# Kernel tuning notes

Measured on AMD Instinct MI355X. Metric: run time of the kernel, lower is better.

The kernel has to match this reference:

```python
import jax, jax.numpy as jnp
import numpy as np


def normalize_adj(adj):
    """Symmetrize (adj + adj.T*(adj.T>adj) - adj*(adj.T>adj)), add self loops, row-normalize D^-1 A."""
    at = jnp.swapaxes(adj, -1, -2)
    mask = (at > adj).astype(adj.dtype)
    a = adj + at * mask - adj * mask
    m = a.shape[-1]
    a = a + jnp.eye(m, dtype=a.dtype)
    rowsum = a.sum(axis=-1, keepdims=True)
    inv = jnp.where(rowsum > 0, 1.0 / rowsum, 0.0)
    return a * inv


def setup_inputs() -> dict:
    key = jax.random.key(0)
    ks = jax.random.split(key, 8)
    N, n, T, dim, M = 4, 3, 512, 2048, 256
    x = jax.random.normal(ks[0], (N, n, T, dim), dtype=jnp.float32)
    nodes = jax.random.normal(ks[1], (N, M, dim), dtype=jnp.float32)
    adj = (jax.random.uniform(ks[2], (N, M, M)) < 0.05).astype(jnp.float32)
    conv_w = jax.random.normal(ks[3], (2048, dim, 3), dtype=jnp.float32) * 0.02  # OIH
    conv_b = jnp.zeros((2048,), dtype=jnp.float32)
    W1 = jax.random.normal(ks[4], (dim, dim), dtype=jnp.float32) * 0.02
    b1 = jnp.zeros((dim,), dtype=jnp.float32)
    W2 = jax.random.normal(ks[5], (dim, dim), dtype=jnp.float32) * 0.02
    b2 = jnp.zeros((dim,), dtype=jnp.float32)
    return {"x": x, "nodes": nodes, "adj": adj, "conv_w": conv_w, "conv_b": conv_b,
            "W1": W1, "b1": b1, "W2": W2, "b2": b2}


def reference(x, nodes, adj, conv_w, conv_b, W1, b1, W2, b2):
    N, n, T, dim = x.shape
    # Conv1d front-end: (N*n, C=dim, T), kernel 3, pad 1, then ReLU
    feats = x.reshape(N * n, T, dim).transpose(0, 2, 1)  # [B, C, T]
    feats = jax.lax.conv_general_dilated(
        feats, conv_w, window_strides=(1,), padding=[(1, 1)],
        dimension_numbers=("NCH", "OIH", "NCH"))
    feats = jax.nn.relu(feats + conv_b[None, :, None])
    feats = feats.transpose(0, 2, 1).reshape(N, n, T, dim)
    # GCN_Module over per-sample node graphs (batched over N)
    a = normalize_adj(adj)                                   # [N, M, M]
    h = jax.nn.relu(jnp.einsum("bij,bjf->bif", a, nodes @ W1) + b1)
    out = jnp.einsum("bij,bjf->bif", a, h @ W2) + b2         # [N, M, dim]
    return feats, out
```

## Files before the change

kernel.cpp:

```cpp
#include <hip/hip_runtime.h>
#include <stdint.h>

typedef __bf16 bf16x8 __attribute__((ext_vector_type(8)));
typedef float floatx4 __attribute__((ext_vector_type(4)));

__device__ __forceinline__ void gload_lds16(const void* g, void* l) {
    __builtin_amdgcn_global_load_lds((const __attribute__((address_space(1))) void*)g,
                                     (__attribute__((address_space(3))) void*)l, 16, 0, 0);
}

__device__ __forceinline__ uint16_t f2bf(float f) {
    uint32_t u = __float_as_uint(f);
    u += 0x7fff + ((u >> 16) & 1);
    return (uint16_t)(u >> 16);
}
__device__ __forceinline__ uint32_t f2bf2(float lo, float hi) {
    return (uint32_t)f2bf(lo) | ((uint32_t)f2bf(hi) << 16);
}

struct AmulSM {
    float vv[256];
    int   jj[256];
    float part[4];
    int   wcnt[4];
    int   woff[4];
    float sinv;
    int   n0;
};

__device__ __forceinline__ void amul_body(const float* __restrict__ adj,
                                          const float* __restrict__ H,
                                          uint16_t* __restrict__ outp,
                                          int b, int i, int tid, AmulSM* sm)
{
    const float* A = adj + ((size_t)b << 16);
    float aij = A[(i << 8) + tid];
    float aji = A[(tid << 8) + i];
    float v = fmaxf(aij, aji);
    if (tid == i) v += 1.0f;

    float s = v;
    #pragma unroll
    for (int off = 32; off > 0; off >>= 1) s += __shfl_down(s, off);

    bool pred = v != 0.0f;
    unsigned long long m = __ballot(pred);
    int wid = tid >> 6;
    if ((tid & 63) == 0) { sm->part[wid] = s; sm->wcnt[wid] = (int)__popcll(m); }
    __syncthreads();
    if (tid == 0) {
        float t = sm->part[0] + sm->part[1] + sm->part[2] + sm->part[3];
        sm->sinv = t > 0.0f ? 1.0f / t : 0.0f;
        int o = 0;
        #pragma unroll
        for (int w = 0; w < 4; ++w) { sm->woff[w] = o; o += sm->wcnt[w]; }
        sm->n0 = o;
    }
    __syncthreads();
    if (pred) {
        int pos = sm->woff[wid] + (int)__popcll(m & ((1ull << (tid & 63)) - 1ull));
        sm->vv[pos] = v * sm->sinv;
        sm->jj[pos] = tid;
    }
    __syncthreads();

    const int n0 = sm->n0;
    const int f0 = tid * 8;
    const float* Hb = H + (((size_t)b) << 8) * 2048;
    float acc[8] = {};
    for (int c = 0; c < n0; ++c) {
        float av = sm->vv[c];
        const float* hp = Hb + (size_t)sm->jj[c] * 2048 + f0;
        float4 p = *(const float4*)hp;
        float4 q = *(const float4*)(hp + 4);
        acc[0] += av * p.x; acc[1] += av * p.y; acc[2] += av * p.z; acc[3] += av * p.w;
        acc[4] += av * q.x; acc[5] += av * q.y; acc[6] += av * q.z; acc[7] += av * q.w;
    }
    uint4 o;
    o.x = f2bf2(acc[0], acc[1]);
    o.y = f2bf2(acc[2], acc[3]);
    o.z = f2bf2(acc[4], acc[5]);
    o.w = f2bf2(acc[6], acc[7]);
    *(uint4*)(outp + (((size_t)b << 8) + i) * 2048 + f0) = o;
}

__device__ __forceinline__ void amul_swizzle(int bid, int& b, int& i) {
    int x = bid & 7, g = bid >> 3;
    b = x >> 1;
    i = ((x & 1) << 7) + g;
}

#define PR_AM 1024
#define PR_W  3072
#define PR_T  5120
#define PR_N  17456

__global__ __launch_bounds__(256)
void k_prep(const float* __restrict__ x, uint16_t* __restrict__ xpad,
            const float* __restrict__ w, uint16_t* __restrict__ wT,
            const float* __restrict__ W1, const float* __restrict__ W2,
            uint16_t* __restrict__ W1T, uint16_t* __restrict__ W2T,
            const float* __restrict__ adj, const float* __restrict__ nodes,
            uint16_t* __restrict__ gbf)
{
    __shared__ union {
        float  wbuf[6144];
        float  tile[64][65];
        AmulSM am;
    } sm;
    const int bid = blockIdx.x;
    const int tid = threadIdx.x;

    if (bid < PR_AM) {
        int b, i; amul_swizzle(bid, b, i);
        amul_body(adj, nodes, gbf, b, i, tid, &sm.am);
    } else if (bid < PR_W) {
        int o = bid - PR_AM;
        const float* src = w + (size_t)o * 6144;
        uint16_t*    dst = wT + (size_t)o * 6144;
        #pragma unroll
        for (int it = 0; it < 24; ++it)
            sm.wbuf[it * 256 + tid] = src[it * 256 + tid];
        __syncthreads();
        #pragma unroll
        for (int h = 0; h < 3; ++h)
            #pragma unroll
            for (int c = 0; c < 8; ++c) {
                int i = c * 256 + tid;
                dst[h * 2048 + i] = f2bf(sm.wbuf[i * 3 + h]);
            }
    } else if (bid < PR_T) {
        int t  = bid - PR_W;
        int z  = t >> 10;
        int by = (t >> 5) & 31;
        int bx = t & 31;
        const float* src = z ? W2 : W1;
        uint16_t*    dst = z ? W2T : W1T;
        int tx = tid & 63, ty = tid >> 6;
        for (int rr = ty; rr < 64; rr += 4)
            sm.tile[rr][tx] = src[(size_t)(by * 64 + rr) * 2048 + bx * 64 + tx];
        __syncthreads();
        for (int rr = ty; rr < 64; rr += 4)
            dst[(size_t)(bx * 64 + rr) * 2048 + by * 64 + tx] = f2bf(sm.tile[tx][rr]);
    } else {
        int idx4 = (bid - PR_T) * 256 + tid;
        int ch4  = idx4 & 511;
        int tmp  = idx4 >> 9;
        int b    = tmp / 514;
        int tt   = tmp - b * 514;
        float4 v = {0.0f, 0.0f, 0.0f, 0.0f};
        if (tt >= 1 && tt <= 512)
            v = *(const float4*)(x + ((size_t)(b * 512 + tt - 1) << 11) + ch4 * 4);
        uint2 o = { f2bf2(v.x, v.y), f2bf2(v.z, v.w) };
        ((uint2*)xpad)[idx4] = o;
    }
}

template<bool RELU>
__device__ __forceinline__ void g64_tile(uint16_t* As, uint16_t* Bs,
                                         const uint16_t* __restrict__ A,
                                         const uint16_t* __restrict__ BT,
                                         float* __restrict__ C, const float* __restrict__ bias,
                                         int rt, int ct)
{
    const int tid  = threadIdx.x;
    const int lane = tid & 63;
    const int wave = tid >> 6;
    const int wm   = (wave >> 1) * 32;
    const int wn   = (wave & 1) * 32;
    const int lm   = lane & 15;
    const int kq   = (lane >> 4) * 8;
    const int sr   = tid >> 2;
    const int sc   = (tid & 3) * 8;

    const size_t abase = (size_t)(rt + sr) * 2048 + sc;
    const size_t bbase = (size_t)(ct + sr) * 2048 + sc;

    floatx4 acc[2][2] = {};

    for (int k0 = 0; k0 < 2048; k0 += 64) {
        #pragma unroll
        for (int p = 0; p < 2; ++p) {
            gload_lds16(A  + abase + k0 + p * 32, &As[p * 2048 + tid * 8]);
            gload_lds16(BT + bbase + k0 + p * 32, &Bs[p * 2048 + tid * 8]);
        }
        __syncthreads();

        #pragma unroll
        for (int s = 0; s < 2; ++s) {
            bf16x8 af[2], bfr[2];
            #pragma unroll
            for (int mt = 0; mt < 2; ++mt)
                af[mt] = *(const bf16x8*)&As[s * 2048 + (wm + mt * 16 + lm) * 32 + kq];
            #pragma unroll
            for (int nt = 0; nt < 2; ++nt)
                bfr[nt] = *(const bf16x8*)&Bs[s * 2048 + (wn + nt * 16 + lm) * 32 + kq];
            #pragma unroll
            for (int mt = 0; mt < 2; ++mt)
                #pragma unroll
                for (int nt = 0; nt < 2; ++nt)
                    acc[mt][nt] = __builtin_amdgcn_mfma_f32_16x16x32_bf16(af[mt], bfr[nt], acc[mt][nt], 0, 0, 0);
        }
        __syncthreads();
    }

    const int lq = lane >> 4;
    #pragma unroll
    for (int mt = 0; mt < 2; ++mt)
        #pragma unroll
        for (int nt = 0; nt < 2; ++nt) {
            int col = ct + wn + nt * 16 + lm;
            float bv = bias[col];
            #pragma unroll
            for (int r = 0; r < 4; ++r) {
                int row = rt + wm + mt * 16 + lq * 4 + r;
                float v = acc[mt][nt][r] + bv;
                if (RELU) v = fmaxf(v, 0.0f);
                C[(size_t)row * 2048 + col] = v;
            }
        }
}

__global__ __launch_bounds__(256)
void k_big(const uint16_t* __restrict__ xpad, const uint16_t* __restrict__ wmT,
           float* __restrict__ feats, const float* __restrict__ conv_b,
           const uint16_t* __restrict__ gbf, const uint16_t* __restrict__ W1T,
           float* __restrict__ h, const float* __restrict__ b1)
{
    __shared__ __align__(16) uint16_t lds[16384];
    const int bid  = blockIdx.x;
    const int tid  = threadIdx.x;
    const int lane = tid & 63;
    const int wave = tid >> 6;
    const int lm   = lane & 15;
    const int kq   = (lane >> 4) * 8;
    const int lq   = lane >> 4;

    if (bid < 768) {
        uint16_t* As = lds;
        uint16_t* Bs = lds + 8192;
        const int xc = bid & 7;
        const int g  = bid >> 3;
        const int rt = (12 * (xc >> 1) + (g % 12)) * 128;
        const int ct = (8 * (xc & 1) + (g / 12)) * 128;
        const int wm = (wave >> 1) * 64;
        const int wn = (wave & 1) * 64;

        const int sr = tid >> 2;
        const int sc = (tid & 3) * 8;
        size_t arow[2]; size_t brow[2];
        #pragma unroll
        for (int rh = 0; rh < 2; ++rh) {
            int r = rt + rh * 64 + sr;
            int b = r >> 9;
            int t = r & 511;
            arow[rh] = ((size_t)(b * 514 + t) << 11);
            brow[rh] = (size_t)(ct + rh * 64 + sr) * 6144;
        }

        floatx4 acc[4][4] = {};

        for (int k0 = 0; k0 < 6144; k0 += 64) {
            const int hh = k0 >> 11;
            const int icb = (k0 & 2047) + sc;
            #pragma unroll
            for (int p = 0; p < 4; ++p) {
                const int s  = p >> 1;
                const int rh = p & 1;
                gload_lds16(xpad + arow[rh] + ((size_t)hh << 11) + icb + s * 32,
                            &As[p * 2048 + tid * 8]);
                gload_lds16(wmT + brow[rh] + k0 + sc + s * 32,
                            &Bs[p * 2048 + tid * 8]);
            }
            __syncthreads();

            #pragma unroll
            for (int s = 0; s < 2; ++s) {
                bf16x8 af[4], bfr[4];
                #pragma unroll
                for (int mt = 0; mt < 4; ++mt)
                    af[mt] = *(const bf16x8*)&As[s * 4096 + (wm + mt * 16 + lm) * 32 + kq];
                #pragma unroll
                for (int nt = 0; nt < 4; ++nt)
                    bfr[nt] = *(const bf16x8*)&Bs[s * 4096 + (wn + nt * 16 + lm) * 32 + kq];
                #pragma unroll
                for (int mt = 0; mt < 4; ++mt)
                    #pragma unroll
                    for (int nt = 0; nt < 4; ++nt)
                        acc[mt][nt] = __builtin_amdgcn_mfma_f32_16x16x32_bf16(af[mt], bfr[nt], acc[mt][nt], 0, 0, 0);
            }
            __syncthreads();
        }

        #pragma unroll
        for (int mt = 0; mt < 4; ++mt)
            #pragma unroll
            for (int nt = 0; nt < 4; ++nt) {
                int col = ct + wn + nt * 16 + lm;
                float bv = conv_b[col];
                #pragma unroll
                for (int r = 0; r < 4; ++r) {
                    int row = rt + wm + mt * 16 + lq * 4 + r;
                    feats[(size_t)row * 2048 + col] = fmaxf(acc[mt][nt][r] + bv, 0.0f);
                }
            }
    } else {
        const int t  = bid - 768;
        const int xc = t & 7;
        const int g  = t >> 3;
        const int rt = (g & 15) * 64;
        const int ct = (4 * xc + (g >> 4)) * 64;
        g64_tile<true>(lds, lds + 4096, gbf, W1T, h, b1, rt, ct);
    }
}

__global__ __launch_bounds__(256)
void k_amul(const float* __restrict__ adj, const float* __restrict__ H,
            uint16_t* __restrict__ outp)
{
    __shared__ AmulSM sm;
    int b, i; amul_swizzle(blockIdx.x, b, i);
    amul_body(adj, H, outp, b, i, threadIdx.x, &sm);
}

__global__ __launch_bounds__(256)
void k_gemm64(const uint16_t* __restrict__ A, const uint16_t* __restrict__ BT,
              float* __restrict__ C, const float* __restrict__ bias)
{
    __shared__ __align__(16) uint16_t lds[8192];
    const int bid = blockIdx.x;
    const int xc  = bid & 7;
    const int g   = bid >> 3;
    const int rt  = (g & 15) * 64;
    const int ct  = (4 * xc + (g >> 4)) * 64;
    g64_tile<false>(lds, lds + 4096, A, BT, C, bias, rt, ct);
}


extern "C" void kernel_launch(void* const* d_in, const int* in_sizes, int n_in,
                              void* d_out, int out_size, void* d_ws, size_t ws_size,
                              hipStream_t stream)
{
    const float* x      = (const float*)d_in[0];
    const float* nodes  = (const float*)d_in[1];
    const float* adj    = (const float*)d_in[2];
    const float* conv_w = (const float*)d_in[3];
    const float* conv_b = (const float*)d_in[4];
    const float* W1     = (const float*)d_in[5];
    const float* b1     = (const float*)d_in[6];
    const float* W2     = (const float*)d_in[7];
    const float* b2     = (const float*)d_in[8];
    float* out = (float*)d_out;

    char* ws = (char*)d_ws;
    uint16_t* xpad   = (uint16_t*)(ws);
    uint16_t* wmT    = (uint16_t*)(ws + 25288704);
    uint16_t* W1T    = (uint16_t*)(ws + 50454528);
    uint16_t* W2T    = (uint16_t*)(ws + 58843136);
    uint16_t* gbf    = (uint16_t*)(ws + 67231744);
    float*    h      = (float*)   (ws + 71426048);
    uint16_t* ahb    = (uint16_t*)(ws + 79814656);

    k_prep<<<PR_N, 256, 0, stream>>>(x, xpad, conv_w, wmT,
                                     W1, W2, W1T, W2T, adj, nodes, gbf);
    k_big<<<1280, 256, 0, stream>>>(xpad, wmT, out, conv_b, gbf, W1T, h, b1);
    k_amul<<<1024, 256, 0, stream>>>(adj, h, ahb);
    k_gemm64<<<512, 256, 0, stream>>>(ahb, W2T, out + 12582912, b2);
}
```

Before: 406.0 us.

## Rewrite conv GEMM as 192x256 tiles with 4-stage LDS pipeline and 8 waves

The conv-as-GEMM part of k_big now uses 512-thread blocks computing 192x256 output tiles over 256 tiles. Operands are staged through a 4-buffer LDS ring with XOR-swizzled layout, explicit vmcnt waits and barriers, and setprio around the MFMA bursts. The aim is to hide global-load latency and raise MFMA utilization compared with the single-buffered 128x128 loop. The W1 GEMM branch now packs two 64x64 tiles per 512-thread block. The cost is 112KB of LDS per block and many more accumulator registers, which may lower occupancy.

```diff
diff --git a/kernel.cpp b/kernel.cpp
--- a/kernel.cpp
+++ b/kernel.cpp
@@ -161,9 +161,8 @@
                                          const uint16_t* __restrict__ A,
                                          const uint16_t* __restrict__ BT,
                                          float* __restrict__ C, const float* __restrict__ bias,
-                                         int rt, int ct)
-{
-    const int tid  = threadIdx.x;
+                                         int rt, int ct, int tid)
+{
     const int lane = tid & 63;
     const int wave = tid >> 6;
     const int wm   = (wave >> 1) * 32;
@@ -221,96 +220,138 @@
         }
 }
 
-__global__ __launch_bounds__(256)
+template<int BUF, bool STG, int VN>
+__device__ __forceinline__ void conv_win(char* ldsb, int tid,
+    const uint16_t*& aS0, const uint16_t*& aS1,
+    const uint16_t*& bS0, const uint16_t*& bS1,
+    int aoff, int boff, floatx4 (&acc)[6][4])
+{
+    char* As  = ldsb + BUF * 12288;
+    char* Bs  = ldsb + 49152 + BUF * 16384;
+    constexpr int NB = (BUF + 3) & 3;
+    char* As3 = ldsb + NB * 12288;
+    char* Bs3 = ldsb + 49152 + NB * 16384;
+
+    bf16x8 av[3], bv[4];
+    #pragma unroll
+    for (int j = 0; j < 3; ++j) av[j] = *(const bf16x8*)(As + aoff + j * 1024);
+    #pragma unroll
+    for (int j = 0; j < 4; ++j) bv[j] = *(const bf16x8*)(Bs + boff + j * 1024);
+    if constexpr (STG) {
+        gload_lds16(aS0, As3 + tid * 16); aS0 += 32;
+        if (tid < 256) { gload_lds16(aS1, As3 + 8192 + tid * 16); aS1 += 32; }
+    }
+    __builtin_amdgcn_s_barrier();
+    asm volatile("s_waitcnt lgkmcnt(0)");
+    __builtin_amdgcn_s_setprio(1);
+    #pragma unroll
+    for (int jm = 0; jm < 3; ++jm)
+        #pragma unroll
+        for (int fn = 0; fn < 4; ++fn)
+            acc[jm][fn] = __builtin_amdgcn_mfma_f32_16x16x32_bf16(av[jm], bv[fn], acc[jm][fn], 0, 0, 0);
+    __builtin_amdgcn_s_setprio(0);
+    __builtin_amdgcn_s_barrier();
+    #pragma unroll
+    for (int j = 0; j < 3; ++j) av[j] = *(const bf16x8*)(As + aoff + 3072 + j * 1024);
+    if constexpr (STG) {
+        gload_lds16(bS0, Bs3 + tid * 16); bS0 += 32;
+        gload_lds16(bS1, Bs3 + 8192 + tid * 16); bS1 += 32;
+    }
+    if constexpr (VN >= 0) asm volatile("s_waitcnt vmcnt(%0)" :: "i"(VN));
+    __builtin_amdgcn_s_barrier();
+    asm volatile("s_waitcnt lgkmcnt(0)");
+    __builtin_amdgcn_s_setprio(1);
+    #pragma unroll
+    for (int jm = 0; jm < 3; ++jm)
+        #pragma unroll
+        for (int fn = 0; fn < 4; ++fn)
+            acc[3 + jm][fn] = __builtin_amdgcn_mfma_f32_16x16x32_bf16(av[jm], bv[fn], acc[3 + jm][fn], 0, 0, 0);
+    __builtin_amdgcn_s_setprio(0);
+    __builtin_amdgcn_s_barrier();
+}
+
+__global__ __launch_bounds__(512, 2)
 void k_big(const uint16_t* __restrict__ xpad, const uint16_t* __restrict__ wmT,
            float* __restrict__ feats, const float* __restrict__ conv_b,
            const uint16_t* __restrict__ gbf, const uint16_t* __restrict__ W1T,
            float* __restrict__ h, const float* __restrict__ b1)
 {
-    __shared__ __align__(16) uint16_t lds[16384];
-    const int bid  = blockIdx.x;
-    const int tid  = threadIdx.x;
-    const int lane = tid & 63;
-    const int wave = tid >> 6;
-    const int lm   = lane & 15;
-    const int kq   = (lane >> 4) * 8;
-    const int lq   = lane >> 4;
-
-    if (bid < 768) {
-        uint16_t* As = lds;
-        uint16_t* Bs = lds + 8192;
-        const int xc = bid & 7;
-        const int g  = bid >> 3;
-        const int rt = (12 * (xc >> 1) + (g % 12)) * 128;
-        const int ct = (8 * (xc & 1) + (g / 12)) * 128;
-        const int wm = (wave >> 1) * 64;
-        const int wn = (wave & 1) * 64;
-
-        const int sr = tid >> 2;
-        const int sc = (tid & 3) * 8;
-        size_t arow[2]; size_t brow[2];
-        #pragma unroll
-        for (int rh = 0; rh < 2; ++rh) {
-            int r = rt + rh * 64 + sr;
-            int b = r >> 9;
-            int t = r & 511;
-            arow[rh] = ((size_t)(b * 514 + t) << 11);
-            brow[rh] = (size_t)(ct + rh * 64 + sr) * 6144;
+    __shared__ __align__(16) char smem[114688];
+    const int bid = blockIdx.x;
+    const int tid = threadIdx.x;
+
+    if (bid < 256) {
+        const int xcd  = bid & 7;
+        const int gg   = bid >> 3;
+        const int tile = xcd * 32 + gg;
+        const int rt   = (tile >> 3) * 192;
+        const int ct   = (tile & 7) * 256;
+
+        const int lane = tid & 63, wave = tid >> 6;
+        const int mw = wave >> 2, nw = wave & 3;
+        const int lm = lane & 15;
+        const int kq2 = (lane >> 4) * 16;
+        const int xc  = kq2 ^ ((lm & 3) << 4);
+        const int aoff = ((mw * 96 + lm) << 6) + xc;
+        const int boff = ((nw * 64 + lm) << 6) + xc;
+
+        const int c1  = 512 + tid;
+        const int r0  = tid >> 2,  kc0 = ((tid & 3) ^ (r0 & 3)) * 8;
+        const int r1  = c1 >> 2,   kc1 = ((c1 & 3) ^ (r1 & 3)) * 8;
+
+        const int RA0 = rt + r0;
+        const int RA1 = rt + r1;
+        const uint16_t* aS0 = xpad + (((size_t)((RA0 >> 9) * 514 + (RA0 & 511))) << 11) + kc0;
+        const uint16_t* aS1 = xpad + (((size_t)((RA1 >> 9) * 514 + (RA1 & 511))) << 11) + kc1;
+        const uint16_t* bS0 = wmT + (size_t)(ct + r0) * 6144 + kc0;
+        const uint16_t* bS1 = wmT + (size_t)(ct + r1) * 6144 + kc1;
+
+        #pragma unroll
+        for (int p = 0; p < 3; ++p) {
+            char* As3 = smem + p * 12288;
+            char* Bs3 = smem + 49152 + p * 16384;
+            gload_lds16(aS0, As3 + tid * 16); aS0 += 32;
+            if (tid < 256) { gload_lds16(aS1, As3 + 8192 + tid * 16); aS1 += 32; }
+            gload_lds16(bS0, Bs3 + tid * 16); bS0 += 32;
+            gload_lds16(bS1, Bs3 + 8192 + tid * 16); bS1 += 32;
         }
-
-        floatx4 acc[4][4] = {};
-
-        for (int k0 = 0; k0 < 6144; k0 += 64) {
-            const int hh = k0 >> 11;
-            const int icb = (k0 & 2047) + sc;
-            #pragma unroll
-            for (int p = 0; p < 4; ++p) {
-                const int s  = p >> 1;
-                const int rh = p & 1;
-                gload_lds16(xpad + arow[rh] + ((size_t)hh << 11) + icb + s * 32,
-                            &As[p * 2048 + tid * 8]);
-                gload_lds16(wmT + brow[rh] + k0 + sc + s * 32,
-                            &Bs[p * 2048 + tid * 8]);
-            }
-            __syncthreads();
-
-            #pragma unroll
-            for (int s = 0; s < 2; ++s) {
-                bf16x8 af[4], bfr[4];
-                #pragma unroll
-                for (int mt = 0; mt < 4; ++mt)
-                    af[mt] = *(const bf16x8*)&As[s * 4096 + (wm + mt * 16 + lm) * 32 + kq];
-                #pragma unroll
-                for (int nt = 0; nt < 4; ++nt)
-                    bfr[nt] = *(const bf16x8*)&Bs[s * 4096 + (wn + nt * 16 + lm) * 32 + kq];
-                #pragma unroll
-                for (int mt = 0; mt < 4; ++mt)
-                    #pragma unroll
-                    for (int nt = 0; nt < 4; ++nt)
-                        acc[mt][nt] = __builtin_amdgcn_mfma_f32_16x16x32_bf16(af[mt], bfr[nt], acc[mt][nt], 0, 0, 0);
-            }
-            __syncthreads();
+        asm volatile("s_waitcnt vmcnt(6)");
+        __builtin_amdgcn_s_barrier();
+
+        floatx4 acc[6][4] = {};
+        #pragma unroll 1
+        for (int it = 0; it < 47; ++it) {
+            conv_win<0, true, 6>(smem, tid, aS0, aS1, bS0, bS1, aoff, boff, acc);
+            conv_win<1, true, 6>(smem, tid, aS0, aS1, bS0, bS1, aoff, boff, acc);
+            conv_win<2, true, 6>(smem, tid, aS0, aS1, bS0, bS1, aoff, boff, acc);
+            conv_win<3, true, 6>(smem, tid, aS0, aS1, bS0, bS1, aoff, boff, acc);
         }
-
-        #pragma unroll
-        for (int mt = 0; mt < 4; ++mt)
-            #pragma unroll
-            for (int nt = 0; nt < 4; ++nt) {
-                int col = ct + wn + nt * 16 + lm;
-                float bv = conv_b[col];
+        conv_win<0, true,  6>(smem, tid, aS0, aS1, bS0, bS1, aoff, boff, acc);
+        conv_win<1, false, 3>(smem, tid, aS0, aS1, bS0, bS1, aoff, boff, acc);
+        conv_win<2, false, 0>(smem, tid, aS0, aS1, bS0, bS1, aoff, boff, acc);
+        conv_win<3, false,-1>(smem, tid, aS0, aS1, bS0, bS1, aoff, boff, acc);
+
+        const int lq = lane >> 4;
+        #pragma unroll
+        for (int fm = 0; fm < 6; ++fm)
+            #pragma unroll
+            for (int fn = 0; fn < 4; ++fn) {
+                int col = ct + nw * 64 + fn * 16 + lm;
+                float bb = conv_b[col];
                 #pragma unroll
                 for (int r = 0; r < 4; ++r) {
-                    int row = rt + wm + mt * 16 + lq * 4 + r;
-                    feats[(size_t)row * 2048 + col] = fmaxf(acc[mt][nt][r] + bv, 0.0f);
+                    int row = rt + mw * 96 + fm * 16 + lq * 4 + r;
+                    feats[(size_t)row * 2048 + col] = fmaxf(acc[fm][fn][r] + bb, 0.0f);
                 }
             }
     } else {
-        const int t  = bid - 768;
-        const int xc = t & 7;
-        const int g  = t >> 3;
-        const int rt = (g & 15) * 64;
-        const int ct = (4 * xc + (g >> 4)) * 64;
-        g64_tile<true>(lds, lds + 4096, gbf, W1T, h, b1, rt, ct);
+        const int t    = bid - 256;
+        const int half = tid >> 8;
+        const int st   = t * 2 + half;
+        const int rt   = (st & 15) * 64;
+        const int ct   = (st >> 4) * 64;
+        uint16_t* As = (uint16_t*)smem + half * 8192;
+        g64_tile<true>(As, As + 4096, gbf, W1T, h, b1, rt, ct, tid & 255);
     }
 }
 
@@ -333,7 +374,7 @@
     const int g   = bid >> 3;
     const int rt  = (g & 15) * 64;
     const int ct  = (4 * xc + (g >> 4)) * 64;
-    g64_tile<false>(lds, lds + 4096, A, BT, C, bias, rt, ct);
+    g64_tile<false>(lds, lds + 4096, A, BT, C, bias, rt, ct, threadIdx.x);
 }
 
 
@@ -363,7 +404,7 @@
 
     k_prep<<<PR_N, 256, 0, stream>>>(x, xpad, conv_w, wmT,
                                      W1, W2, W1T, W2T, adj, nodes, gbf);
-    k_big<<<1280, 256, 0, stream>>>(xpad, wmT, out, conv_b, gbf, W1T, h, b1);
+    k_big<<<512, 512, 0, stream>>>(xpad, wmT, out, conv_b, gbf, W1T, h, b1);
     k_amul<<<1024, 256, 0, stream>>>(adj, h, ahb);
     k_gemm64<<<512, 256, 0, stream>>>(ahb, W2T, out + 12582912, b2);
 }
```

Result: faster. 389.2 us (-4.1%).

## Double-buffer conv GEMM with 192x256 tiles and swizzled LDS; enlarge GCN tiles

Applied to the files above, without the earlier changes.

The conv GEMM becomes a double-buffered pipeline using 192x256 block tiles, XOR-swizzled LDS layout, explicit vmcnt waits, raw barriers and setprio around MFMA bursts, so there are 256 large tiles instead of 768 128x128 ones. The GCN GEMMs switch from 64x64 to 128x128 tiles with swizzled LDS. Grid sizes shrink accordingly. This is meant to hide global-load latency, cut LDS bank conflicts and raise arithmetic intensity. The cost is higher register and LDS pressure, and with fewer blocks the GPU may be less evenly filled, including the tail where the GCN blocks run.

```diff
diff --git a/kernel.cpp b/kernel.cpp
--- a/kernel.cpp
+++ b/kernel.cpp
@@ -3,6 +3,8 @@
 
 typedef __bf16 bf16x8 __attribute__((ext_vector_type(8)));
 typedef float floatx4 __attribute__((ext_vector_type(4)));
+
+#define SB0 __builtin_amdgcn_sched_barrier(0)
 
 __device__ __forceinline__ void gload_lds16(const void* g, void* l) {
     __builtin_amdgcn_global_load_lds((const __attribute__((address_space(1))) void*)g,
@@ -157,58 +159,57 @@
 }
 
 template<bool RELU>
-__device__ __forceinline__ void g64_tile(uint16_t* As, uint16_t* Bs,
-                                         const uint16_t* __restrict__ A,
-                                         const uint16_t* __restrict__ BT,
-                                         float* __restrict__ C, const float* __restrict__ bias,
-                                         int rt, int ct)
-{
-    const int tid  = threadIdx.x;
-    const int lane = tid & 63;
-    const int wave = tid >> 6;
-    const int wm   = (wave >> 1) * 32;
-    const int wn   = (wave & 1) * 32;
-    const int lm   = lane & 15;
-    const int kq   = (lane >> 4) * 8;
-    const int sr   = tid >> 2;
-    const int sc   = (tid & 3) * 8;
-
-    const size_t abase = (size_t)(rt + sr) * 2048 + sc;
-    const size_t bbase = (size_t)(ct + sr) * 2048 + sc;
-
-    floatx4 acc[2][2] = {};
-
+__device__ __forceinline__ void g128_tile(char* lds, const uint16_t* __restrict__ A,
+                                          const uint16_t* __restrict__ BT,
+                                          float* __restrict__ C, const float* __restrict__ bias,
+                                          int rt, int ct, int tid)
+{
+    char* As = lds;
+    char* Bs = lds + 16384;
+    const int lane = tid & 63, wave = tid >> 6;
+    const int wm = (wave >> 1) * 64, wn = (wave & 1) * 64;
+    const int lm = lane & 15, lq = lane >> 4;
+    const int abyte = (wm + lm) * 64 + ((lq * 16) ^ ((lm & 3) << 4));
+    const int bbyte = (wn + lm) * 64 + ((lq * 16) ^ ((lm & 3) << 4));
+
+    int soff[4];
+    #pragma unroll
+    for (int j = 0; j < 4; ++j) {
+        int c = tid + 256 * j;
+        int row = (c >> 2) & 127;
+        soff[j] = row * 2048 + ((c >> 9) << 5) + (((c & 3) ^ (row & 3)) << 3);
+    }
+
+    floatx4 acc[4][4] = {};
     for (int k0 = 0; k0 < 2048; k0 += 64) {
         #pragma unroll
-        for (int p = 0; p < 2; ++p) {
-            gload_lds16(A  + abase + k0 + p * 32, &As[p * 2048 + tid * 8]);
-            gload_lds16(BT + bbase + k0 + p * 32, &Bs[p * 2048 + tid * 8]);
+        for (int j = 0; j < 4; ++j) {
+            gload_lds16(A  + (size_t)rt * 2048 + soff[j] + k0, As + tid * 16 + j * 4096);
+            gload_lds16(BT + (size_t)ct * 2048 + soff[j] + k0, Bs + tid * 16 + j * 4096);
         }
         __syncthreads();
-
         #pragma unroll
         for (int s = 0; s < 2; ++s) {
-            bf16x8 af[2], bfr[2];
-            #pragma unroll
-            for (int mt = 0; mt < 2; ++mt)
-                af[mt] = *(const bf16x8*)&As[s * 2048 + (wm + mt * 16 + lm) * 32 + kq];
-            #pragma unroll
-            for (int nt = 0; nt < 2; ++nt)
-                bfr[nt] = *(const bf16x8*)&Bs[s * 2048 + (wn + nt * 16 + lm) * 32 + kq];
-            #pragma unroll
-            for (int mt = 0; mt < 2; ++mt)
+            bf16x8 af[4], bfr[4];
+            #pragma unroll
+            for (int mt = 0; mt < 4; ++mt)
+                af[mt] = *(const bf16x8*)(As + s * 8192 + abyte + mt * 1024);
+            #pragma unroll
+            for (int nt = 0; nt < 4; ++nt)
+                bfr[nt] = *(const bf16x8*)(Bs + s * 8192 + bbyte + nt * 1024);
+            #pragma unroll
+            for (int mt = 0; mt < 4; ++mt)
                 #pragma unroll
-                for (int nt = 0; nt < 2; ++nt)
+                for (int nt = 0; nt < 4; ++nt)
                     acc[mt][nt] = __builtin_amdgcn_mfma_f32_16x16x32_bf16(af[mt], bfr[nt], acc[mt][nt], 0, 0, 0);
         }
         __syncthreads();
     }
 
-    const int lq = lane >> 4;
-    #pragma unroll
-    for (int mt = 0; mt < 2; ++mt)
-        #pragma unroll
-        for (int nt = 0; nt < 2; ++nt) {
+    #pragma unroll
+    for (int mt = 0; mt < 4; ++mt)
+        #pragma unroll
+        for (int nt = 0; nt < 4; ++nt) {
             int col = ct + wn + nt * 16 + lm;
             float bv = bias[col];
             #pragma unroll
@@ -221,96 +222,126 @@
         }
 }
 
-__global__ __launch_bounds__(256)
+template<int CUR, bool STG, int VN>
+__device__ __forceinline__ void conv_w2(char* smem, int tid,
+    const uint16_t* (&aP)[3], const uint16_t* (&bP)[4],
+    int abase, int bbase, floatx4 (&acc)[6][8])
+{
+    char* As  = smem + CUR * 12288;
+    char* Bs  = smem + 24576 + CUR * 16384;
+    char* Asn = smem + (CUR ^ 1) * 12288;
+    char* Bsn = smem + 24576 + (CUR ^ 1) * 16384;
+
+    if constexpr (STG) {
+        #pragma unroll
+        for (int j = 0; j < 3; ++j) { gload_lds16(aP[j], Asn + tid * 16 + j * 4096); aP[j] += 32; }
+        #pragma unroll
+        for (int j = 0; j < 4; ++j) { gload_lds16(bP[j], Bsn + tid * 16 + j * 4096); bP[j] += 32; }
+    }
+    SB0;
+    asm volatile("s_waitcnt vmcnt(%0)" :: "i"(VN));
+    SB0;
+    __builtin_amdgcn_s_barrier();
+    SB0;
+
+    bf16x8 bv[8], av[3];
+    #pragma unroll
+    for (int fn = 0; fn < 8; ++fn) bv[fn] = *(const bf16x8*)(Bs + bbase + fn * 1024);
+    #pragma unroll
+    for (int fm = 0; fm < 3; ++fm) av[fm] = *(const bf16x8*)(As + abase + fm * 1024);
+    __builtin_amdgcn_s_setprio(1);
+    #pragma unroll
+    for (int fm = 0; fm < 3; ++fm)
+        #pragma unroll
+        for (int fn = 0; fn < 8; ++fn)
+            acc[fm][fn] = __builtin_amdgcn_mfma_f32_16x16x32_bf16(av[fm], bv[fn], acc[fm][fn], 0, 0, 0);
+    __builtin_amdgcn_s_setprio(0);
+    #pragma unroll
+    for (int fm = 0; fm < 3; ++fm) av[fm] = *(const bf16x8*)(As + abase + 3072 + fm * 1024);
+    __builtin_amdgcn_s_setprio(1);
+    #pragma unroll
+    for (int fm = 0; fm < 3; ++fm)
+        #pragma unroll
+        for (int fn = 0; fn < 8; ++fn)
+            acc[3 + fm][fn] = __builtin_amdgcn_mfma_f32_16x16x32_bf16(av[fm], bv[fn], acc[3 + fm][fn], 0, 0, 0);
+    __builtin_amdgcn_s_setprio(0);
+    SB0;
+    __builtin_amdgcn_s_barrier();
+    SB0;
+}
+
+__global__ __launch_bounds__(256, 2)
 void k_big(const uint16_t* __restrict__ xpad, const uint16_t* __restrict__ wmT,
            float* __restrict__ feats, const float* __restrict__ conv_b,
            const uint16_t* __restrict__ gbf, const uint16_t* __restrict__ W1T,
            float* __restrict__ h, const float* __restrict__ b1)
 {
-    __shared__ __align__(16) uint16_t lds[16384];
-    const int bid  = blockIdx.x;
-    const int tid  = threadIdx.x;
-    const int lane = tid & 63;
-    const int wave = tid >> 6;
-    const int lm   = lane & 15;
-    const int kq   = (lane >> 4) * 8;
-    const int lq   = lane >> 4;
-
-    if (bid < 768) {
-        uint16_t* As = lds;
-        uint16_t* Bs = lds + 8192;
-        const int xc = bid & 7;
-        const int g  = bid >> 3;
-        const int rt = (12 * (xc >> 1) + (g % 12)) * 128;
-        const int ct = (8 * (xc & 1) + (g / 12)) * 128;
-        const int wm = (wave >> 1) * 64;
-        const int wn = (wave & 1) * 64;
-
-        const int sr = tid >> 2;
-        const int sc = (tid & 3) * 8;
-        size_t arow[2]; size_t brow[2];
-        #pragma unroll
-        for (int rh = 0; rh < 2; ++rh) {
-            int r = rt + rh * 64 + sr;
-            int b = r >> 9;
-            int t = r & 511;
-            arow[rh] = ((size_t)(b * 514 + t) << 11);
-            brow[rh] = (size_t)(ct + rh * 64 + sr) * 6144;
-        }
-
-        floatx4 acc[4][4] = {};
-
-        for (int k0 = 0; k0 < 6144; k0 += 64) {
-            const int hh = k0 >> 11;
-            const int icb = (k0 & 2047) + sc;
-            #pragma unroll
-            for (int p = 0; p < 4; ++p) {
-                const int s  = p >> 1;
-                const int rh = p & 1;
-                gload_lds16(xpad + arow[rh] + ((size_t)hh << 11) + icb + s * 32,
-                            &As[p * 2048 + tid * 8]);
-                gload_lds16(wmT + brow[rh] + k0 + sc + s * 32,
-                            &Bs[p * 2048 + tid * 8]);
-            }
-            __syncthreads();
-
-            #pragma unroll
-            for (int s = 0; s < 2; ++s) {
-                bf16x8 af[4], bfr[4];
-                #pragma unroll
-                for (int mt = 0; mt < 4; ++mt)
-                    af[mt] = *(const bf16x8*)&As[s * 4096 + (wm + mt * 16 + lm) * 32 + kq];
-                #pragma unroll
-                for (int nt = 0; nt < 4; ++nt)
-                    bfr[nt] = *(const bf16x8*)&Bs[s * 4096 + (wn + nt * 16 + lm) * 32 + kq];
-                #pragma unroll
-                for (int mt = 0; mt < 4; ++mt)
-                    #pragma unroll
-                    for (int nt = 0; nt < 4; ++nt)
-                        acc[mt][nt] = __builtin_amdgcn_mfma_f32_16x16x32_bf16(af[mt], bfr[nt], acc[mt][nt], 0, 0, 0);
-            }
-            __syncthreads();
-        }
-
-        #pragma unroll
-        for (int mt = 0; mt < 4; ++mt)
-            #pragma unroll
-            for (int nt = 0; nt < 4; ++nt) {
-                int col = ct + wn + nt * 16 + lm;
-                float bv = conv_b[col];
+    __shared__ __align__(16) char smem[57344];
+    const int bid = blockIdx.x;
+    const int tid = threadIdx.x;
+
+    if (bid < 256) {
+        const int xcd  = bid & 7;
+        const int gg   = bid >> 3;
+        const int tile = xcd * 32 + gg;
+        const int rt   = (tile >> 3) * 192;
+        const int ct   = (tile & 7) * 256;
+
+        const int lane = tid & 63, wave = tid >> 6;
+        const int mw = wave >> 1, nw = wave & 1;
+        const int lm = lane & 15, lq = lane >> 4;
+        const int abase = (mw * 96 + lm) * 64 + ((lq * 16) ^ ((lm & 3) << 4));
+        const int bbase = (nw * 128 + lm) * 64 + ((lq * 16) ^ ((lm & 3) << 4));
+
+        const uint16_t* aP[3];
+        const uint16_t* bP[4];
+        #pragma unroll
+        for (int j = 0; j < 3; ++j) {
+            int c = tid + 256 * j;
+            int row = c >> 2;
+            int R = rt + row;
+            aP[j] = xpad + (((size_t)((R >> 9) * 514 + (R & 511))) << 11)
+                         + (((c & 3) ^ (row & 3)) << 3);
+        }
+        #pragma unroll
+        for (int j = 0; j < 4; ++j) {
+            int c = tid + 256 * j;
+            int row = c >> 2;
+            bP[j] = wmT + (size_t)(ct + row) * 6144 + (((c & 3) ^ (row & 3)) << 3);
+        }
+
+        #pragma unroll
+        for (int j = 0; j < 3; ++j) { gload_lds16(aP[j], smem + tid * 16 + j * 4096); aP[j] += 32; }
+        #pragma unroll
+        for (int j = 0; j < 4; ++j) { gload_lds16(bP[j], smem + 24576 + tid * 16 + j * 4096); bP[j] += 32; }
+
+        floatx4 acc[6][8] = {};
+        #pragma unroll 1
+        for (int it = 0; it < 95; ++it) {
+            conv_w2<0, true, 7>(smem, tid, aP, bP, abase, bbase, acc);
+            conv_w2<1, true, 7>(smem, tid, aP, bP, abase, bbase, acc);
+        }
+        conv_w2<0, true, 7>(smem, tid, aP, bP, abase, bbase, acc);
+        conv_w2<1, false, 0>(smem, tid, aP, bP, abase, bbase, acc);
+
+        #pragma unroll
+        for (int fm = 0; fm < 6; ++fm)
+            #pragma unroll
+            for (int fn = 0; fn < 8; ++fn) {
+                int col = ct + nw * 128 + fn * 16 + lm;
+                float bb = conv_b[col];
                 #pragma unroll
                 for (int r = 0; r < 4; ++r) {
-                    int row = rt + wm + mt * 16 + lq * 4 + r;
-                    feats[(size_t)row * 2048 + col] = fmaxf(acc[mt][nt][r] + bv, 0.0f);
+                    int row = rt + mw * 96 + fm * 16 + lq * 4 + r;
+                    feats[(size_t)row * 2048 + col] = fmaxf(acc[fm][fn][r] + bb, 0.0f);
                 }
             }
     } else {
-        const int t  = bid - 768;
-        const int xc = t & 7;
-        const int g  = t >> 3;
-        const int rt = (g & 15) * 64;
-        const int ct = (4 * xc + (g >> 4)) * 64;
-        g64_tile<true>(lds, lds + 4096, gbf, W1T, h, b1, rt, ct);
+        const int t   = bid - 256;
+        const int idx = (t & 7) * 16 + (t >> 3);
+        const int rt  = (idx & 7) * 128;
+        const int ct  = (idx >> 3) * 128;
+        g128_tile<true>(smem, gbf, W1T, h, b1, rt, ct, tid);
     }
 }
 
@@ -327,13 +358,12 @@
 void k_gemm64(const uint16_t* __restrict__ A, const uint16_t* __restrict__ BT,
               float* __restrict__ C, const float* __restrict__ bias)
 {
-    __shared__ __align__(16) uint16_t lds[8192];
+    __shared__ __align__(16) char lds[32768];
     const int bid = blockIdx.x;
-    const int xc  = bid & 7;
-    const int g   = bid >> 3;
-    const int rt  = (g & 15) * 64;
-    const int ct  = (4 * xc + (g >> 4)) * 64;
-    g64_tile<false>(lds, lds + 4096, A, BT, C, bias, rt, ct);
+    const int idx = (bid & 7) * 16 + (bid >> 3);
+    const int rt  = (idx & 7) * 128;
+    const int ct  = (idx >> 3) * 128;
+    g128_tile<false>(lds, A, BT, C, bias, rt, ct, threadIdx.x);
 }
 
 
@@ -363,7 +393,7 @@
 
     k_prep<<<PR_N, 256, 0, stream>>>(x, xpad, conv_w, wmT,
                                      W1, W2, W1T, W2T, adj, nodes, gbf);
-    k_big<<<1280, 256, 0, stream>>>(xpad, wmT, out, conv_b, gbf, W1T, h, b1);
+    k_big<<<384, 256, 0, stream>>>(xpad, wmT, out, conv_b, gbf, W1T, h, b1);
     k_amul<<<1024, 256, 0, stream>>>(adj, h, ahb);
-    k_gemm64<<<512, 256, 0, stream>>>(ahb, W2T, out + 12582912, b2);
-}
+    k_gemm64<<<128, 256, 0, stream>>>(ahb, W2T, out + 12582912, b2);
+}
```

Measured after the change: 479.3 us. 18.1% more time.
